# Kernel optimization log

Measured on AMD Instinct MI355X. Metric: run time of the kernel, lower is better.

Reference implementation:

```python
import jax, jax.numpy as jnp
import numpy as np

B, S, D = 8, 2048, 512

def setup_inputs() -> dict:
    key = jax.random.key(0)
    ks = jax.random.split(key, 9)
    scale = 1.0 / np.sqrt(D)
    return {
        "x": jax.random.normal(ks[0], (B, S, D), dtype=jnp.float32),
        "attention_mask": jax.random.uniform(ks[1], (B, S), dtype=jnp.float32),
        "Wq": jax.random.normal(ks[2], (D, D), dtype=jnp.float32) * scale,
        "bq": jax.random.normal(ks[3], (D,), dtype=jnp.float32) * 0.01,
        "Wk": jax.random.normal(ks[4], (D, D), dtype=jnp.float32) * scale,
        "bk": jax.random.normal(ks[5], (D,), dtype=jnp.float32) * 0.01,
        "Wv": jax.random.normal(ks[6], (D, D), dtype=jnp.float32) * scale,
        "bv": jax.random.normal(ks[7], (D,), dtype=jnp.float32) * 0.01,
    }

def reference(x, attention_mask, Wq, bq, Wk, bk, Wv, bv):
    # Single-head self-attention, full O(S^2) scores as in the original.
    q = jnp.einsum('bsd,df->bsf', x, Wq) + bq  # [B,S,D]
    k = jnp.einsum('bsd,df->bsf', x, Wk) + bk
    v = jnp.einsum('bsd,df->bsf', x, Wv) + bv
    scores = jnp.einsum('bqd,bkd->bqk', q, k) / jnp.sqrt(jnp.float32(D))  # [B,S,S]
    attn = jax.nn.softmax(scores, axis=2)
    weighted = jnp.einsum('bqk,bkd->bqd', attn, v)  # [B,S,D]
    # mask applied multiplicatively to the output, per original code
    return weighted * attention_mask[:, :, None]
```

## Files before the change

### kernel.cpp

```cpp
#include <hip/hip_runtime.h>
#include <math.h>
#include <stdint.h>


typedef _Float16 f16x8 __attribute__((ext_vector_type(8)));
typedef _Float16 f16x4 __attribute__((ext_vector_type(4)));
typedef _Float16 f16x2 __attribute__((ext_vector_type(2)));
typedef float f32x4 __attribute__((ext_vector_type(4)));

__device__ __forceinline__ void async16(const _Float16* g, _Float16* l) {
    __builtin_amdgcn_global_load_lds(
        (const __attribute__((address_space(1))) unsigned int*)(uintptr_t)g,
        (__attribute__((address_space(3))) unsigned int*)(unsigned int)(uintptr_t)l,
        16, 0, 0);
}

__device__ __forceinline__ float frag_sum8(f16x8 v, float acc) {
#if __has_builtin(__builtin_amdgcn_fdot2)
    const f16x2 one2 = {(_Float16)1.f, (_Float16)1.f};
    const f16x2* p = (const f16x2*)&v;
    acc = __builtin_amdgcn_fdot2(p[0], one2, acc, false);
    acc = __builtin_amdgcn_fdot2(p[1], one2, acc, false);
    acc = __builtin_amdgcn_fdot2(p[2], one2, acc, false);
    acc = __builtin_amdgcn_fdot2(p[3], one2, acc, false);
#else
#pragma unroll
    for (int j = 0; j < 8; j++) acc += (float)v[j];
#endif
    return acc;
}

#define MFMA16(a, b, c) __builtin_amdgcn_mfma_f32_16x16x32_f16(a, b, c, 0, 0, 0)
#define BAR() __builtin_amdgcn_s_barrier()
#define LGKM0() asm volatile("s_waitcnt lgkmcnt(0)" ::: "memory")

template <int NT, bool WITH_RS>
__device__ __forceinline__ void core8w(
    const _Float16* __restrict__ A, const _Float16* __restrict__ B,
    int ld, int row0, int col0, _Float16* sm, f32x4 acc[4][2], float rs[4])
{
    const int tid = threadIdx.x, lane = tid & 63, wave = tid >> 6;
    const int wm = wave >> 2, wn = wave & 3;
    const int rc = lane >> 3;
    const int swz = ((lane & 7) ^ rc) * 8;
    const int fr = lane & 15, q = lane >> 4, fx = fr & 7;
    const size_t laneoff = (size_t)rc * ld + swz;

    const int ah0c = (wave & 3) + (wave >> 2) * 8;
    const int ah1c = ah0c + 4;
    const int b0c = 2 * wave, b1c = b0c + 1;
    const _Float16* gAh0 = A + (size_t)(row0 + 8 * ah0c) * ld + laneoff;
    const _Float16* gAh1 = A + (size_t)(row0 + 8 * ah1c) * ld + laneoff;
    const _Float16* gB0  = B + (size_t)(col0 + 8 * b0c) * ld + laneoff;
    const _Float16* gB1  = B + (size_t)(col0 + 8 * b1c) * ld + laneoff;
    const int lAh0 = ah0c * 512, lAh1 = ah1c * 512;
    const int lB0 = 8192 + b0c * 512, lB1 = 8192 + b1c * 512;

    async16(gAh0, sm + lAh0);
    async16(gAh1, sm + lAh1);
    async16(gB0,  sm + lB0);
    async16(gB1,  sm + lB1);
    async16(gB0 + 64,  sm + 16384 + lB0);
    async16(gB1 + 64,  sm + 16384 + lB1);
    async16(gAh0 + 64, sm + 16384 + lAh0);
    asm volatile("s_waitcnt vmcnt(3)" ::: "memory");
    BAR();

#pragma unroll 2
    for (int t = 0; t < NT; ++t) {
        const _Float16* As = sm + (t & 1) * 16384;
        const _Float16* Bs = As + 8192;
        f16x8 af[2][2], bf[2][2];

#pragma unroll
        for (int m = 0; m < 2; m++)
#pragma unroll
            for (int s = 0; s < 2; s++) {
                int ra = wm * 64 + m * 16 + fr;
                af[m][s] = *(const f16x8*)&As[ra * 64 + (((s * 4 + q) ^ fx) * 8)];
            }
#pragma unroll
        for (int n = 0; n < 2; n++)
#pragma unroll
            for (int s = 0; s < 2; s++) {
                int rb = wn * 32 + n * 16 + fr;
                bf[n][s] = *(const f16x8*)&Bs[rb * 64 + (((s * 4 + q) ^ fx) * 8)];
            }
        if (t + 1 < NT)
            async16(gAh1 + (t + 1) * 64, sm + ((t + 1) & 1) * 16384 + lAh1);
        BAR(); LGKM0();
        if (WITH_RS) {
#pragma unroll
            for (int m = 0; m < 2; m++)
#pragma unroll
                for (int s = 0; s < 2; s++) rs[m] = frag_sum8(af[m][s], rs[m]);
        }
        __builtin_amdgcn_s_setprio(1);
#pragma unroll
        for (int s = 0; s < 2; s++)
#pragma unroll
            for (int m = 0; m < 2; m++)
#pragma unroll
                for (int n = 0; n < 2; n++)
                    acc[m][n] = MFMA16(af[m][s], bf[n][s], acc[m][n]);
        __builtin_amdgcn_s_setprio(0);
        BAR();

#pragma unroll
        for (int m = 0; m < 2; m++)
#pragma unroll
            for (int s = 0; s < 2; s++) {
                int ra = wm * 64 + (2 + m) * 16 + fr;
                af[m][s] = *(const f16x8*)&As[ra * 64 + (((s * 4 + q) ^ fx) * 8)];
            }
        if (t + 2 < NT) {
            _Float16* stg = sm + (t & 1) * 16384;
            const int k2 = (t + 2) * 64;
            async16(gB0 + k2,  stg + lB0);
            async16(gB1 + k2,  stg + lB1);
            async16(gAh0 + k2, stg + lAh0);
        }
        BAR(); LGKM0();
        if (WITH_RS) {
#pragma unroll
            for (int m = 0; m < 2; m++)
#pragma unroll
                for (int s = 0; s < 2; s++) rs[2 + m] = frag_sum8(af[m][s], rs[2 + m]);
        }
        __builtin_amdgcn_s_setprio(1);
#pragma unroll
        for (int s = 0; s < 2; s++)
#pragma unroll
            for (int m = 0; m < 2; m++)
#pragma unroll
                for (int n = 0; n < 2; n++)
                    acc[2 + m][n] = MFMA16(af[m][s], bf[n][s], acc[2 + m][n]);
        __builtin_amdgcn_s_setprio(0);
        if (t + 2 < NT) {
            asm volatile("s_waitcnt vmcnt(3)" ::: "memory");
        } else {
            asm volatile("s_waitcnt vmcnt(0)" ::: "memory");
        }
        BAR();
    }
}

__global__ __launch_bounds__(256) void prep(
    const float* __restrict__ x,
    const float* __restrict__ Wq, const float* __restrict__ Wk,
    const float* __restrict__ Wv,
    _Float16* __restrict__ Xh,
    _Float16* __restrict__ WqT, _Float16* __restrict__ WkT,
    _Float16* __restrict__ WvT)
{
    const int bid = blockIdx.x;
    if (bid < 8192) {
        int i = (bid * 256 + threadIdx.x) * 4;
        float4 v = *(const float4*)(x + i);
        f16x4 h;
        h.x = (_Float16)v.x; h.y = (_Float16)v.y;
        h.z = (_Float16)v.z; h.w = (_Float16)v.w;
        *(f16x4*)&Xh[i] = h;
    } else {
        int t = bid - 8192;
        int z = t >> 10;
        const float* W = (z == 0) ? Wq : (z == 1) ? Wk : Wv;
        _Float16* Wt   = (z == 0) ? WqT : (z == 1) ? WkT : WvT;
        int idx = (t & 1023) * 256 + threadIdx.x;
        int n = idx >> 9, k = idx & 511;
        Wt[idx] = (_Float16)W[k * 512 + n];
    }
}

__global__ __launch_bounds__(512, 4) void proj_mfma(
    const _Float16* __restrict__ Xh,
    const _Float16* __restrict__ WqT, const float* __restrict__ bq,
    const _Float16* __restrict__ WkT, const float* __restrict__ bk,
    const _Float16* __restrict__ WvT, const float* __restrict__ bv,
    _Float16* __restrict__ Qh, _Float16* __restrict__ Kh,
    _Float16* __restrict__ Vt)
{
    __shared__ __align__(16) _Float16 smem[2 * 16384];
    const int z = blockIdx.z;
    f32x4 acc[4][2];
#pragma unroll
    for (int i = 0; i < 4; i++)
#pragma unroll
        for (int j = 0; j < 2; j++) acc[i][j] = (f32x4){0.f, 0.f, 0.f, 0.f};
    float rs_unused[4];

    const int lane = threadIdx.x & 63, wave = threadIdx.x >> 6;
    const int wm = wave >> 2, wn = wave & 3;
    const int er = (lane >> 4) * 4, ec = lane & 15;

    if (z < 2) {
        const _Float16* Wt = (z == 0) ? WqT : WkT;
        const float* bias  = (z == 0) ? bq : bk;
        _Float16* P        = (z == 0) ? Qh : Kh;
        const float sc     = (z == 0) ? 0.04419417382415922f : 1.0f;
        const int row0 = blockIdx.x * 128, col0 = blockIdx.y * 128;
        core8w<8, false>(Xh, Wt, 512, row0, col0, smem, acc, rs_unused);
#pragma unroll
        for (int tm = 0; tm < 4; tm++)
#pragma unroll
            for (int tn = 0; tn < 2; tn++) {
                int col = col0 + wn * 32 + tn * 16 + ec;
                float bb = bias[col];
#pragma unroll
                for (int r = 0; r < 4; r++) {
                    int row = row0 + wm * 64 + tm * 16 + er + r;
                    P[(size_t)row * 512 + col] = (_Float16)((acc[tm][tn][r] + bb) * sc);
                }
            }
    } else {
        const int row0 = blockIdx.y * 128;
        const int col0 = blockIdx.x * 128;
        core8w<8, false>(WvT, Xh, 512, row0, col0, smem, acc, rs_unused);
#pragma unroll
        for (int tm = 0; tm < 4; tm++)
#pragma unroll
            for (int tn = 0; tn < 2; tn++) {
                int col = col0 + wn * 32 + tn * 16 + ec;
                size_t obase = (size_t)(col >> 11) * (512 * 2048) + (col & 2047);
#pragma unroll
                for (int r = 0; r < 4; r++) {
                    int row = row0 + wm * 64 + tm * 16 + er + r;
                    Vt[obase + (size_t)row * 2048] = (_Float16)(acc[tm][tn][r] + bv[row]);
                }
            }
    }
}

__global__ __launch_bounds__(512, 4) void scores_mfma(
    const _Float16* __restrict__ Qh, const _Float16* __restrict__ Kh,
    _Float16* __restrict__ Sh)
{
    __shared__ __align__(16) _Float16 smem[2 * 16384];
    const int bid = blockIdx.x;
    const int b   = bid & 7;
    const int rem = bid >> 3;
    const int col0 = (rem & 15) * 128;
    const int row0 = (rem >> 4) * 128;

    const _Float16* A = Qh + (size_t)b * 2048 * 512;
    const _Float16* B = Kh + (size_t)b * 2048 * 512;
    _Float16* S = Sh + (size_t)b * 2048 * 2048;

    f32x4 acc[4][2];
#pragma unroll
    for (int i = 0; i < 4; i++)
#pragma unroll
        for (int j = 0; j < 2; j++) acc[i][j] = (f32x4){0.f, 0.f, 0.f, 0.f};
    float rs_unused[4];

    core8w<8, false>(A, B, 512, row0, col0, smem, acc, rs_unused);

    const int lane = threadIdx.x & 63, wave = threadIdx.x >> 6;
    const int wm = wave >> 2, wn = wave & 3;
    const int er = (lane >> 4) * 4, ec = lane & 15;
#pragma unroll
    for (int tm = 0; tm < 4; tm++)
#pragma unroll
        for (int tn = 0; tn < 2; tn++) {
            int col = col0 + wn * 32 + tn * 16 + ec;
#pragma unroll
            for (int r = 0; r < 4; r++) {
                int row = row0 + wm * 64 + tm * 16 + er + r;
                S[(size_t)row * 2048 + col] = (_Float16)__expf(acc[tm][tn][r]);
            }
        }
}

__global__ __launch_bounds__(512, 4) void av_mfma(
    const _Float16* __restrict__ Sh, const _Float16* __restrict__ Vt,
    const float* __restrict__ mask, float* __restrict__ out)
{
    __shared__ __align__(16) _Float16 smem[2 * 16384];
    const int bid = blockIdx.x;
    const int b   = bid & 7;
    const int rem = bid >> 3;
    const int col0 = (rem & 3) * 128;
    const int row0 = (rem >> 2) * 128;

    const _Float16* A = Sh + (size_t)b * 2048 * 2048;
    const _Float16* B = Vt + (size_t)b * 512 * 2048;
    float* O = out + (size_t)b * 2048 * 512;
    const float* mk = mask + (size_t)b * 2048;

    f32x4 acc[4][2];
#pragma unroll
    for (int i = 0; i < 4; i++)
#pragma unroll
        for (int j = 0; j < 2; j++) acc[i][j] = (f32x4){0.f, 0.f, 0.f, 0.f};
    float rs[4] = {0.f, 0.f, 0.f, 0.f};

    core8w<32, true>(A, B, 2048, row0, col0, smem, acc, rs);

    const int lane = threadIdx.x & 63, wave = threadIdx.x >> 6;
    const int wm = wave >> 2, wn = wave & 3;
    const int er = (lane >> 4) * 4, ec = lane & 15;

#pragma unroll
    for (int tm = 0; tm < 4; tm++) {
        rs[tm] += __shfl_xor(rs[tm], 16, 64);
        rs[tm] += __shfl_xor(rs[tm], 32, 64);
    }
    __syncthreads();
    float* l_s = (float*)smem;
    if (wn == 0 && lane < 16) {
#pragma unroll
        for (int tm = 0; tm < 4; tm++) l_s[wm * 64 + tm * 16 + lane] = rs[tm];
    }
    __syncthreads();

#pragma unroll
    for (int tm = 0; tm < 4; tm++)
#pragma unroll
        for (int r = 0; r < 4; r++) {
            int lrow = wm * 64 + tm * 16 + er + r;
            int row = row0 + lrow;
            float s = mk[row] / l_s[lrow];
#pragma unroll
            for (int tn = 0; tn < 2; tn++) {
                int col = col0 + wn * 32 + tn * 16 + ec;
                O[(size_t)row * 512 + col] = acc[tm][tn][r] * s;
            }
        }
}

extern "C" void kernel_launch(void* const* d_in, const int* in_sizes, int n_in,
                              void* d_out, int out_size, void* d_ws, size_t ws_size,
                              hipStream_t stream) {
    const float* x    = (const float*)d_in[0];
    const float* mask = (const float*)d_in[1];
    const float* Wq   = (const float*)d_in[2];
    const float* bq   = (const float*)d_in[3];
    const float* Wk   = (const float*)d_in[4];
    const float* bk   = (const float*)d_in[5];
    const float* Wv   = (const float*)d_in[6];
    const float* bv   = (const float*)d_in[7];
    float* out = (float*)d_out;

    const size_t BSD = (size_t)8 * 2048 * 512;
    _Float16* base = (_Float16*)d_ws;
    _Float16* Qh  = base;
    _Float16* Kh  = Qh + BSD;
    _Float16* Vt  = Kh + BSD;
    _Float16* WqT = Vt + BSD;
    _Float16* WkT = WqT + 512 * 512;
    _Float16* WvT = WkT + 512 * 512;
    _Float16* Xh  = WvT + 512 * 512;
    _Float16* Sh  = Xh;

    prep<<<dim3(8192 + 3 * 1024), dim3(256), 0, stream>>>(
        x, Wq, Wk, Wv, Xh, WqT, WkT, WvT);
    proj_mfma<<<dim3(128, 4, 3), dim3(512), 0, stream>>>(
        Xh, WqT, bq, WkT, bk, WvT, bv, Qh, Kh, Vt);
    scores_mfma<<<dim3(2048), dim3(512), 0, stream>>>(Qh, Kh, Sh);
    av_mfma<<<dim3(512), dim3(512), 0, stream>>>(Sh, Vt, mask, out);
}
```

Baseline: 246.2 us.

## Shrink GEMM block tiles to 128x64 with four-wave blocks

Replaces the 8-wave 128x128 tiled GEMM core with a 4-wave 128x64 variant used by the projection, scores and AV kernels. Each wave now loads more A chunks and the LDS double buffer shrinks, and grid sizes double to cover the outputs. This is meant to give more blocks for occupancy and load balance across CUs, at the cost of lower data reuse per block (A is loaded twice as often) and more global traffic.

```diff
diff --git a/kernel.cpp b/kernel.cpp
--- a/kernel.cpp
+++ b/kernel.cpp
@@ -35,40 +35,44 @@
 #define LGKM0() asm volatile("s_waitcnt lgkmcnt(0)" ::: "memory")
 
 template <int NT, bool WITH_RS>
-__device__ __forceinline__ void core8w(
+__device__ __forceinline__ void core64(
     const _Float16* __restrict__ A, const _Float16* __restrict__ B,
     int ld, int row0, int col0, _Float16* sm, f32x4 acc[4][2], float rs[4])
 {
+    constexpr int BUFH = 12288;
     const int tid = threadIdx.x, lane = tid & 63, wave = tid >> 6;
-    const int wm = wave >> 2, wn = wave & 3;
+    const int wm = wave >> 1, wn = wave & 1;
     const int rc = lane >> 3;
     const int swz = ((lane & 7) ^ rc) * 8;
     const int fr = lane & 15, q = lane >> 4, fx = fr & 7;
     const size_t laneoff = (size_t)rc * ld + swz;
 
-    const int ah0c = (wave & 3) + (wave >> 2) * 8;
-    const int ah1c = ah0c + 4;
-    const int b0c = 2 * wave, b1c = b0c + 1;
-    const _Float16* gAh0 = A + (size_t)(row0 + 8 * ah0c) * ld + laneoff;
-    const _Float16* gAh1 = A + (size_t)(row0 + 8 * ah1c) * ld + laneoff;
-    const _Float16* gB0  = B + (size_t)(col0 + 8 * b0c) * ld + laneoff;
-    const _Float16* gB1  = B + (size_t)(col0 + 8 * b1c) * ld + laneoff;
-    const int lAh0 = ah0c * 512, lAh1 = ah1c * 512;
-    const int lB0 = 8192 + b0c * 512, lB1 = 8192 + b1c * 512;
-
-    async16(gAh0, sm + lAh0);
-    async16(gAh1, sm + lAh1);
-    async16(gB0,  sm + lB0);
-    async16(gB1,  sm + lB1);
-    async16(gB0 + 64,  sm + 16384 + lB0);
-    async16(gB1 + 64,  sm + 16384 + lB1);
-    async16(gAh0 + 64, sm + 16384 + lAh0);
-    asm volatile("s_waitcnt vmcnt(3)" ::: "memory");
+    const int c00 = wave, c01 = 8 + wave;
+    const int c10 = 4 + wave, c11 = 12 + wave;
+    const int cb0 = 2 * wave, cb1 = 2 * wave + 1;
+    const _Float16* gA00 = A + (size_t)(row0 + 8 * c00) * ld + laneoff;
+    const _Float16* gA01 = A + (size_t)(row0 + 8 * c01) * ld + laneoff;
+    const _Float16* gA10 = A + (size_t)(row0 + 8 * c10) * ld + laneoff;
+    const _Float16* gA11 = A + (size_t)(row0 + 8 * c11) * ld + laneoff;
+    const _Float16* gB0  = B + (size_t)(col0 + 8 * cb0) * ld + laneoff;
+    const _Float16* gB1  = B + (size_t)(col0 + 8 * cb1) * ld + laneoff;
+    const int l00 = c00 * 512, l01 = c01 * 512;
+    const int l10 = c10 * 512, l11 = c11 * 512;
+    const int lB0 = 8192 + cb0 * 512, lB1 = 8192 + cb1 * 512;
+
+    async16(gA00, sm + l00);  async16(gA01, sm + l01);
+    async16(gA10, sm + l10);  async16(gA11, sm + l11);
+    async16(gB0,  sm + lB0);  async16(gB1,  sm + lB1);
+    async16(gA00 + 64, sm + BUFH + l00);
+    async16(gA01 + 64, sm + BUFH + l01);
+    async16(gB0 + 64,  sm + BUFH + lB0);
+    async16(gB1 + 64,  sm + BUFH + lB1);
+    asm volatile("s_waitcnt vmcnt(4)" ::: "memory");
     BAR();
 
 #pragma unroll 2
     for (int t = 0; t < NT; ++t) {
-        const _Float16* As = sm + (t & 1) * 16384;
+        const _Float16* As = sm + (t & 1) * BUFH;
         const _Float16* Bs = As + 8192;
         f16x8 af[2][2], bf[2][2];
 
@@ -86,8 +90,12 @@
                 int rb = wn * 32 + n * 16 + fr;
                 bf[n][s] = *(const f16x8*)&Bs[rb * 64 + (((s * 4 + q) ^ fx) * 8)];
             }
-        if (t + 1 < NT)
-            async16(gAh1 + (t + 1) * 64, sm + ((t + 1) & 1) * 16384 + lAh1);
+        if (t + 1 < NT) {
+            _Float16* nb = sm + ((t + 1) & 1) * BUFH;
+            const int k1 = (t + 1) * 64;
+            async16(gA10 + k1, nb + l10);
+            async16(gA11 + k1, nb + l11);
+        }
         BAR(); LGKM0();
         if (WITH_RS) {
 #pragma unroll
@@ -114,11 +122,12 @@
                 af[m][s] = *(const f16x8*)&As[ra * 64 + (((s * 4 + q) ^ fx) * 8)];
             }
         if (t + 2 < NT) {
-            _Float16* stg = sm + (t & 1) * 16384;
+            _Float16* stg = sm + (t & 1) * BUFH;
             const int k2 = (t + 2) * 64;
+            async16(gA00 + k2, stg + l00);
+            async16(gA01 + k2, stg + l01);
             async16(gB0 + k2,  stg + lB0);
             async16(gB1 + k2,  stg + lB1);
-            async16(gAh0 + k2, stg + lAh0);
         }
         BAR(); LGKM0();
         if (WITH_RS) {
@@ -137,7 +146,7 @@
                     acc[2 + m][n] = MFMA16(af[m][s], bf[n][s], acc[2 + m][n]);
         __builtin_amdgcn_s_setprio(0);
         if (t + 2 < NT) {
-            asm volatile("s_waitcnt vmcnt(3)" ::: "memory");
+            asm volatile("s_waitcnt vmcnt(4)" ::: "memory");
         } else {
             asm volatile("s_waitcnt vmcnt(0)" ::: "memory");
         }
@@ -172,7 +181,7 @@
     }
 }
 
-__global__ __launch_bounds__(512, 4) void proj_mfma(
+__global__ __launch_bounds__(256, 3) void proj_mfma(
     const _Float16* __restrict__ Xh,
     const _Float16* __restrict__ WqT, const float* __restrict__ bq,
     const _Float16* __restrict__ WkT, const float* __restrict__ bk,
@@ -180,7 +189,7 @@
     _Float16* __restrict__ Qh, _Float16* __restrict__ Kh,
     _Float16* __restrict__ Vt)
 {
-    __shared__ __align__(16) _Float16 smem[2 * 16384];
+    __shared__ __align__(16) _Float16 smem[2 * 12288];
     const int z = blockIdx.z;
     f32x4 acc[4][2];
 #pragma unroll
@@ -190,7 +199,7 @@
     float rs_unused[4];
 
     const int lane = threadIdx.x & 63, wave = threadIdx.x >> 6;
-    const int wm = wave >> 2, wn = wave & 3;
+    const int wm = wave >> 1, wn = wave & 1;
     const int er = (lane >> 4) * 4, ec = lane & 15;
 
     if (z < 2) {
@@ -198,8 +207,8 @@
         const float* bias  = (z == 0) ? bq : bk;
         _Float16* P        = (z == 0) ? Qh : Kh;
         const float sc     = (z == 0) ? 0.04419417382415922f : 1.0f;
-        const int row0 = blockIdx.x * 128, col0 = blockIdx.y * 128;
-        core8w<8, false>(Xh, Wt, 512, row0, col0, smem, acc, rs_unused);
+        const int row0 = blockIdx.x * 128, col0 = blockIdx.y * 64;
+        core64<8, false>(Xh, Wt, 512, row0, col0, smem, acc, rs_unused);
 #pragma unroll
         for (int tm = 0; tm < 4; tm++)
 #pragma unroll
@@ -213,9 +222,10 @@
                 }
             }
     } else {
-        const int row0 = blockIdx.y * 128;
-        const int col0 = blockIdx.x * 128;
-        core8w<8, false>(WvT, Xh, 512, row0, col0, smem, acc, rs_unused);
+        const int idx = blockIdx.y * 128 + blockIdx.x;
+        const int row0 = (idx >> 8) * 128;
+        const int col0 = (idx & 255) * 64;
+        core64<8, false>(WvT, Xh, 512, row0, col0, smem, acc, rs_unused);
 #pragma unroll
         for (int tm = 0; tm < 4; tm++)
 #pragma unroll
@@ -231,16 +241,16 @@
     }
 }
 
-__global__ __launch_bounds__(512, 4) void scores_mfma(
+__global__ __launch_bounds__(256, 3) void scores_mfma(
     const _Float16* __restrict__ Qh, const _Float16* __restrict__ Kh,
     _Float16* __restrict__ Sh)
 {
-    __shared__ __align__(16) _Float16 smem[2 * 16384];
+    __shared__ __align__(16) _Float16 smem[2 * 12288];
     const int bid = blockIdx.x;
     const int b   = bid & 7;
     const int rem = bid >> 3;
-    const int col0 = (rem & 15) * 128;
-    const int row0 = (rem >> 4) * 128;
+    const int col0 = (rem & 31) * 64;
+    const int row0 = (rem >> 5) * 128;
 
     const _Float16* A = Qh + (size_t)b * 2048 * 512;
     const _Float16* B = Kh + (size_t)b * 2048 * 512;
@@ -253,10 +263,10 @@
         for (int j = 0; j < 2; j++) acc[i][j] = (f32x4){0.f, 0.f, 0.f, 0.f};
     float rs_unused[4];
 
-    core8w<8, false>(A, B, 512, row0, col0, smem, acc, rs_unused);
+    core64<8, false>(A, B, 512, row0, col0, smem, acc, rs_unused);
 
     const int lane = threadIdx.x & 63, wave = threadIdx.x >> 6;
-    const int wm = wave >> 2, wn = wave & 3;
+    const int wm = wave >> 1, wn = wave & 1;
     const int er = (lane >> 4) * 4, ec = lane & 15;
 #pragma unroll
     for (int tm = 0; tm < 4; tm++)
@@ -271,16 +281,16 @@
         }
 }
 
-__global__ __launch_bounds__(512, 4) void av_mfma(
+__global__ __launch_bounds__(256, 3) void av_mfma(
     const _Float16* __restrict__ Sh, const _Float16* __restrict__ Vt,
     const float* __restrict__ mask, float* __restrict__ out)
 {
-    __shared__ __align__(16) _Float16 smem[2 * 16384];
+    __shared__ __align__(16) _Float16 smem[2 * 12288];
     const int bid = blockIdx.x;
     const int b   = bid & 7;
     const int rem = bid >> 3;
-    const int col0 = (rem & 3) * 128;
-    const int row0 = (rem >> 2) * 128;
+    const int col0 = (rem & 7) * 64;
+    const int row0 = (rem >> 3) * 128;
 
     const _Float16* A = Sh + (size_t)b * 2048 * 2048;
     const _Float16* B = Vt + (size_t)b * 512 * 2048;
@@ -294,10 +304,10 @@
         for (int j = 0; j < 2; j++) acc[i][j] = (f32x4){0.f, 0.f, 0.f, 0.f};
     float rs[4] = {0.f, 0.f, 0.f, 0.f};
 
-    core8w<32, true>(A, B, 2048, row0, col0, smem, acc, rs);
+    core64<32, true>(A, B, 2048, row0, col0, smem, acc, rs);
 
     const int lane = threadIdx.x & 63, wave = threadIdx.x >> 6;
-    const int wm = wave >> 2, wn = wave & 3;
+    const int wm = wave >> 1, wn = wave & 1;
     const int er = (lane >> 4) * 4, ec = lane & 15;
 
 #pragma unroll
@@ -354,8 +364,8 @@
 
     prep<<<dim3(8192 + 3 * 1024), dim3(256), 0, stream>>>(
         x, Wq, Wk, Wv, Xh, WqT, WkT, WvT);
-    proj_mfma<<<dim3(128, 4, 3), dim3(512), 0, stream>>>(
+    proj_mfma<<<dim3(128, 8, 3), dim3(256), 0, stream>>>(
         Xh, WqT, bq, WkT, bk, WvT, bv, Qh, Kh, Vt);
-    scores_mfma<<<dim3(2048), dim3(512), 0, stream>>>(Qh, Kh, Sh);
-    av_mfma<<<dim3(512), dim3(512), 0, stream>>>(Sh, Vt, mask, out);
-}
+    scores_mfma<<<dim3(4096), dim3(256), 0, stream>>>(Qh, Kh, Sh);
+    av_mfma<<<dim3(1024), dim3(256), 0, stream>>>(Sh, Vt, mask, out);
+}
```

After: 230.9 us. -6.2%, faster.
